# Performance work log

Measured on AMD Instinct MI355X. Metric: run time of the kernel, lower is better.

Reference implementation:

```python
import jax, jax.numpy as jnp
import numpy as np

N_NODES = 50000


def setup_inputs() -> dict:
    key = jax.random.key(0)
    ks = jax.random.split(key, 9)
    d = 256
    E = 800000
    inp = {
        "x": jax.random.normal(ks[0], (N_NODES, d), dtype=jnp.float32),
        "edge_index": jax.random.randint(ks[1], (2, E), 0, N_NODES, dtype=jnp.int64),
    }
    # 3 GCNConv layers, each: weight [in, out] and bias [out] (Glorot-ish scale)
    scale = 1.0 / np.sqrt(d)
    for i in range(3):
        inp[f"W{i+1}"] = jax.random.normal(ks[2 + 2 * i], (d, d), dtype=jnp.float32) * scale
        inp[f"b{i+1}"] = jnp.zeros((d,), dtype=jnp.float32)
    return inp


def _gcn_conv(h, src, dst, norm, W, b, n_nodes):
    # linear transform then normalized gather-scatter aggregation
    h = h @ W                                   # [N, out]
    msg = h[src] * norm[:, None]                # [E+N, out]
    out = jax.ops.segment_sum(msg, dst, num_segments=n_nodes)
    return out + b


def reference(x, edge_index, W1, b1, W2, b2, W3, b3):
    n = x.shape[0]
    loop = jnp.arange(n, dtype=edge_index.dtype)
    src = jnp.concatenate([edge_index[0], loop])  # add self-loops
    dst = jnp.concatenate([edge_index[1], loop])
    # symmetric normalization: deg^{-1/2}[src] * deg^{-1/2}[dst]
    deg = jax.ops.segment_sum(jnp.ones_like(dst, dtype=x.dtype), dst, num_segments=n)
    dinv = jnp.where(deg > 0, jax.lax.rsqrt(deg), 0.0)
    norm = dinv[src] * dinv[dst]

    h = _gcn_conv(x, src, dst, norm, W1, b1, n)
    h = jax.nn.relu(h)
    h = _gcn_conv(h, src, dst, norm, W2, b2, n)
    h = jax.nn.relu(h)
    h = _gcn_conv(h, src, dst, norm, W3, b3, n)
    return h
```

## Files before the change

kernel.cpp:

```cpp
#include <hip/hip_runtime.h>
#include <math.h>


using bf16x8  = __attribute__((ext_vector_type(8))) short;
using ushort4v = __attribute__((ext_vector_type(4))) unsigned short;
using f32x4   = __attribute__((ext_vector_type(4))) float;
using half4   = __attribute__((ext_vector_type(4))) _Float16;

__device__ inline unsigned short f2bf(float v) {
    union { float f; unsigned u; } x; x.f = v;
    unsigned r = x.u + 0x7fff + ((x.u >> 16) & 1);
    return (unsigned short)(r >> 16);
}
__device__ inline float bf2f(unsigned short b) {
    union { float f; unsigned u; } x; x.u = ((unsigned)b) << 16;
    return x.f;
}
__device__ inline unsigned short f2h_bits(float v) {
    _Float16 h = (_Float16)v;
    union { _Float16 h; unsigned short u; } c; c.h = h;
    return c.u;
}


__global__ void hist_kernel(const int* __restrict__ dst, int E, int* __restrict__ cnt) {
    int e = blockIdx.x * blockDim.x + threadIdx.x;
    if (e < E) atomicAdd(&cnt[dst[e]], 1);
}

__global__ void scan_block_kernel(const int* __restrict__ in, int n,
                                  int* __restrict__ out, int* __restrict__ bsums) {
    __shared__ int s[256];
    int t = threadIdx.x;
    int i = blockIdx.x * 256 + t;
    s[t] = (i < n) ? in[i] : 0;
    __syncthreads();
    for (int off = 1; off < 256; off <<= 1) {
        int addv = (t >= off) ? s[t - off] : 0;
        __syncthreads();
        s[t] += addv;
        __syncthreads();
    }
    if (i < n) out[i] = s[t];
    if (t == 255) bsums[blockIdx.x] = s[255];
}

__global__ void scan_sums_kernel(int* __restrict__ bsums, int nb) {
    __shared__ int s[256];
    int t = threadIdx.x;
    s[t] = (t < nb) ? bsums[t] : 0;
    __syncthreads();
    for (int off = 1; off < 256; off <<= 1) {
        int addv = (t >= off) ? s[t - off] : 0;
        __syncthreads();
        s[t] += addv;
        __syncthreads();
    }
    if (t < nb) bsums[t] = s[t];
}

__global__ void scan_add_dinv_kernel(int* __restrict__ scn, int n, const int* __restrict__ bsums,
                                     const int* __restrict__ cnt, float* __restrict__ dinv,
                                     int* __restrict__ cursor) {
    int i = blockIdx.x * 256 + threadIdx.x;
    if (i < n) {
        int s = scn[i] + (blockIdx.x > 0 ? bsums[blockIdx.x - 1] : 0);
        scn[i] = s;
        int c = cnt[i];
        dinv[i] = rsqrtf((float)(c + 1));
        cursor[i] = s - c;
    }
}

__global__ void scatter_kernel(const int* __restrict__ src, const int* __restrict__ dst, int E,
                               const float* __restrict__ dinv, int* __restrict__ cursor,
                               int* __restrict__ ssrc, float* __restrict__ snorm) {
    int e = blockIdx.x * blockDim.x + threadIdx.x;
    if (e < E) {
        int s = src[e], d0 = dst[e];
        int pos = atomicAdd(&cursor[d0], 1);
        ssrc[pos] = s;
        snorm[pos] = dinv[s] * dinv[d0];
    }
}

__global__ __launch_bounds__(256) void wsplit3_kernel(const float* __restrict__ Wa,
                                                      const float* __restrict__ Wb,
                                                      const float* __restrict__ Wc,
                                                      unsigned short* __restrict__ Wsp) {
    __shared__ float t[64][65];
    int w = blockIdx.z;
    const float* W = (w == 0) ? Wa : (w == 1) ? Wb : Wc;
    int k0 = blockIdx.x * 64, n0 = blockIdx.y * 64;
    int tid = threadIdx.x;
    int r = tid >> 6, c = tid & 63;
#pragma unroll
    for (int i = 0; i < 16; ++i) {
        int kk = i * 4 + r;
        t[kk][c] = W[(size_t)(k0 + kk) * 256 + n0 + c];
    }
    __syncthreads();
    unsigned short* Hi = Wsp + (size_t)w * 131072;
    unsigned short* Lo = Hi + 65536;
#pragma unroll
    for (int i = 0; i < 16; ++i) {
        int nn = i * 4 + r;
        float v = t[c][nn];
        unsigned short h = f2bf(v);
        unsigned short l2 = f2bf(v - bf2f(h));
        Hi[(size_t)(n0 + nn) * 256 + k0 + c] = h;
        Lo[(size_t)(n0 + nn) * 256 + k0 + c] = l2;
    }
}

__global__ void xsplit_kernel(const float* __restrict__ in, unsigned short* __restrict__ hi,
                              unsigned short* __restrict__ lo, int total4) {
    int i = blockIdx.x * blockDim.x + threadIdx.x;
    int stride = gridDim.x * blockDim.x;
    for (; i < total4; i += stride) {
        float4 v = ((const float4*)in)[i];
        ushort4v h, l;
        h[0] = f2bf(v.x); l[0] = f2bf(v.x - bf2f(h[0]));
        h[1] = f2bf(v.y); l[1] = f2bf(v.y - bf2f(h[1]));
        h[2] = f2bf(v.z); l[2] = f2bf(v.z - bf2f(h[2]));
        h[3] = f2bf(v.w); l[3] = f2bf(v.w - bf2f(h[3]));
        ((ushort4v*)hi)[i] = h;
        ((ushort4v*)lo)[i] = l;
    }
}

__global__ __launch_bounds__(256) void gemm_ps_kernel(
        const unsigned short* __restrict__ Ahi, const unsigned short* __restrict__ Alo,
        const unsigned short* __restrict__ Bht, const unsigned short* __restrict__ Blt,
        unsigned short* __restrict__ C16, int M) {
    __shared__ unsigned short lds[32768];

    const int tid  = threadIdx.x;
    const int lane = tid & 63;
    const int wid  = tid >> 6;
    const int wr   = wid >> 1, wc = wid & 1;

    const int orig = blockIdx.x;
    const int xcd  = orig & 7;
    const int idx  = orig >> 3;
    const int wg   = (xcd < 6 ? xcd * 98 : 588 + (xcd - 6) * 97) + idx;
    const int mBase = (wg >> 1) * 128;
    const int nBase = (wg & 1) * 128;

    const int b0 = (lane ^ (lane >> 2) ^ (lane >> 4)) & 1;
    const int b1 = ((lane >> 1) ^ (lane >> 3)) & 1;
    const int b2 = ((lane >> 2) ^ (lane >> 4)) & 1;
    const int g  = (lane & 0x38) | (b2 << 2) | (b1 << 1) | b0;
    const int srow = g >> 2;
    const int skg  = g & 3;

    const unsigned short* gbase =
        (wid == 0) ? Ahi : (wid == 1) ? Alo : (wid == 2) ? Bht : Blt;
    const int rowbase = (wid < 2) ? mBase : nBase;

    int grows[8];
#pragma unroll
    for (int c = 0; c < 8; ++c) {
        int r = rowbase + c * 16 + srow;
        if (wid < 2 && r >= M) r = M - 1;
        grows[c] = r;
    }

    f32x4 acc[4][4];
#pragma unroll
    for (int i = 0; i < 4; ++i)
#pragma unroll
        for (int j = 0; j < 4; ++j) acc[i][j] = (f32x4){0.f, 0.f, 0.f, 0.f};

    auto stage = [&](int p, int k) {
        unsigned short* ldsw = lds + p * 16384 + wid * 4096;
        const int k0 = k * 32;
#pragma unroll
        for (int c = 0; c < 8; ++c) {
            const unsigned short* ga = gbase + (size_t)grows[c] * 256 + k0 + skg * 8;
            __builtin_amdgcn_global_load_lds(
                (const __attribute__((address_space(1))) void*)ga,
                (__attribute__((address_space(3))) void*)(ldsw + c * 512),
                16, 0, 0);
        }
    };

    stage(0, 0);

#pragma unroll
    for (int k = 0; k < 8; ++k) {
        const int p = k & 1;
        if (k < 7) {
            stage(p ^ 1, k + 1);
            asm volatile("s_waitcnt vmcnt(8)" ::: "memory");
        } else {
            asm volatile("s_waitcnt vmcnt(0)" ::: "memory");
        }
        __builtin_amdgcn_s_barrier();

        const unsigned short* Ah = lds + p * 16384;
        const unsigned short* Al = Ah + 4096;
        const unsigned short* Bh = Ah + 8192;
        const unsigned short* Bl = Ah + 12288;

        const int kb = (lane >> 4) * 8;
        bf16x8 fah[4], fal[4], fbh[4], fbl[4];
#pragma unroll
        for (int mi = 0; mi < 4; ++mi) {
            int row = wr * 64 + mi * 16 + (lane & 15);
            int off = (row * 64 + kb * 2) ^ ((row & 7) << 4);
            fah[mi] = *(const bf16x8*)((const char*)Ah + off);
            fal[mi] = *(const bf16x8*)((const char*)Al + off);
        }
#pragma unroll
        for (int ni = 0; ni < 4; ++ni) {
            int col = wc * 64 + ni * 16 + (lane & 15);
            int off = (col * 64 + kb * 2) ^ ((col & 7) << 4);
            fbh[ni] = *(const bf16x8*)((const char*)Bh + off);
            fbl[ni] = *(const bf16x8*)((const char*)Bl + off);
        }
#pragma unroll
        for (int mi = 0; mi < 4; ++mi)
#pragma unroll
            for (int ni = 0; ni < 4; ++ni) {
                acc[mi][ni] = __builtin_amdgcn_mfma_f32_16x16x32_bf16(
                    fah[mi], fbh[ni], acc[mi][ni], 0, 0, 0);
                acc[mi][ni] = __builtin_amdgcn_mfma_f32_16x16x32_bf16(
                    fah[mi], fbl[ni], acc[mi][ni], 0, 0, 0);
                acc[mi][ni] = __builtin_amdgcn_mfma_f32_16x16x32_bf16(
                    fal[mi], fbh[ni], acc[mi][ni], 0, 0, 0);
            }
        __builtin_amdgcn_s_barrier();
    }

#pragma unroll
    for (int mi = 0; mi < 4; ++mi) {
        int row0 = mBase + wr * 64 + mi * 16 + (lane >> 4) * 4;
#pragma unroll
        for (int ni = 0; ni < 4; ++ni) {
            int col = nBase + wc * 64 + ni * 16 + (lane & 15);
#pragma unroll
            for (int r = 0; r < 4; ++r) {
                int row = row0 + r;
                if (row < M) C16[(size_t)row * 256 + col] = f2h_bits(acc[mi][ni][r]);
            }
        }
    }
}

template <int RELU, int SPLIT>
__global__ __launch_bounds__(256) void agg_kernel(const unsigned short* __restrict__ hH,
                                                  const int* __restrict__ ssrc,
                                                  const float* __restrict__ snorm,
                                                  const int* __restrict__ cnt,
                                                  const int* __restrict__ scanv,
                                                  const float* __restrict__ dinv,
                                                  const float* __restrict__ bias,
                                                  unsigned short* __restrict__ outHi,
                                                  unsigned short* __restrict__ outLo,
                                                  float* __restrict__ outF, int n) {
    int node = blockIdx.x * 4 + (threadIdx.x >> 6);
    int lane = threadIdx.x & 63;
    if (node >= n) return;
    int end = scanv[node];
    int start = end - cnt[node];
    float di = dinv[node];
    float wself = di * di;

    half4 v = ((const half4*)(hH + (size_t)node * 256))[lane];
    float ax = (float)v[0] * wself, ay = (float)v[1] * wself;
    float az = (float)v[2] * wself, aw = (float)v[3] * wself;

    int j = start;
    for (; j + 4 <= end; j += 4) {
        int s0 = ssrc[j], s1 = ssrc[j + 1], s2 = ssrc[j + 2], s3 = ssrc[j + 3];
        float w0 = snorm[j], w1 = snorm[j + 1], w2 = snorm[j + 2], w3 = snorm[j + 3];
        half4 u0 = ((const half4*)(hH + (size_t)s0 * 256))[lane];
        half4 u1 = ((const half4*)(hH + (size_t)s1 * 256))[lane];
        half4 u2 = ((const half4*)(hH + (size_t)s2 * 256))[lane];
        half4 u3 = ((const half4*)(hH + (size_t)s3 * 256))[lane];
        ax = fmaf((float)u0[0], w0, ax); ay = fmaf((float)u0[1], w0, ay);
        az = fmaf((float)u0[2], w0, az); aw = fmaf((float)u0[3], w0, aw);
        ax = fmaf((float)u1[0], w1, ax); ay = fmaf((float)u1[1], w1, ay);
        az = fmaf((float)u1[2], w1, az); aw = fmaf((float)u1[3], w1, aw);
        ax = fmaf((float)u2[0], w2, ax); ay = fmaf((float)u2[1], w2, ay);
        az = fmaf((float)u2[2], w2, az); aw = fmaf((float)u2[3], w2, aw);
        ax = fmaf((float)u3[0], w3, ax); ay = fmaf((float)u3[1], w3, ay);
        az = fmaf((float)u3[2], w3, az); aw = fmaf((float)u3[3], w3, aw);
    }
    for (; j < end; ++j) {
        int s = ssrc[j];
        float wn = snorm[j];
        half4 u = ((const half4*)(hH + (size_t)s * 256))[lane];
        ax = fmaf((float)u[0], wn, ax); ay = fmaf((float)u[1], wn, ay);
        az = fmaf((float)u[2], wn, az); aw = fmaf((float)u[3], wn, aw);
    }

    float4 bb = ((const float4*)bias)[lane];
    ax += bb.x; ay += bb.y; az += bb.z; aw += bb.w;
    if (RELU) {
        ax = fmaxf(ax, 0.0f); ay = fmaxf(ay, 0.0f);
        az = fmaxf(az, 0.0f); aw = fmaxf(aw, 0.0f);
    }
    if (SPLIT) {
        ushort4v h, l;
        h[0] = f2bf(ax); l[0] = f2bf(ax - bf2f(h[0]));
        h[1] = f2bf(ay); l[1] = f2bf(ay - bf2f(h[1]));
        h[2] = f2bf(az); l[2] = f2bf(az - bf2f(h[2]));
        h[3] = f2bf(aw); l[3] = f2bf(aw - bf2f(h[3]));
        ((ushort4v*)(outHi + (size_t)node * 256))[lane] = h;
        ((ushort4v*)(outLo + (size_t)node * 256))[lane] = l;
    } else {
        float4 o = {ax, ay, az, aw};
        ((float4*)(outF + (size_t)node * 256))[lane] = o;
    }
}

extern "C" void kernel_launch(void* const* d_in, const int* in_sizes, int n_in,
                              void* d_out, int out_size, void* d_ws, size_t ws_size,
                              hipStream_t stream) {
    const float* x  = (const float*)d_in[0];
    const int*   ei = (const int*)d_in[1];
    const float* W1 = (const float*)d_in[2];
    const float* b1 = (const float*)d_in[3];
    const float* W2 = (const float*)d_in[4];
    const float* b2 = (const float*)d_in[5];
    const float* W3 = (const float*)d_in[6];
    const float* b3 = (const float*)d_in[7];

    const int n = in_sizes[0] / 256;
    const int E = in_sizes[1] / 2;
    const int* src = ei;
    const int* dst = ei + E;

    unsigned short* Hi = (unsigned short*)d_out;
    unsigned short* Lo = Hi + (size_t)n * 256;
    float* outF = (float*)d_out;

    char* ws = (char*)d_ws;
    unsigned short* hH = (unsigned short*)ws;
    size_t off  = (size_t)n * 256 * 2;
    off = (off + 255) & ~(size_t)255;
    float* dinv = (float*)(ws + off); off += (size_t)n * 4;
    int*   cnt  = (int*)(ws + off);   off += (size_t)n * 4;
    int*   scn  = (int*)(ws + off);   off += (size_t)n * 4;
    int*   cur  = (int*)(ws + off);   off += (size_t)n * 4;
    int*   bsum = (int*)(ws + off);   off += 4096;
    int*   ssrc = (int*)(ws + off);   off += (size_t)E * 4;
    float* snrm = (float*)(ws + off); off += (size_t)E * 4;
    off = (off + 255) & ~(size_t)255;
    unsigned short* Wsp = (unsigned short*)(ws + off);
    off += (size_t)3 * 2 * 65536 * 2;

    hipMemsetAsync(cnt, 0, (size_t)n * 4, stream);

    const int eb = (E + 255) / 256;
    const int nb = (n + 255) / 256;

    wsplit3_kernel<<<dim3(4, 4, 3), 256, 0, stream>>>(W1, W2, W3, Wsp);
    xsplit_kernel<<<2048, 256, 0, stream>>>(x, Hi, Lo, n * 64);

    hist_kernel<<<eb, 256, 0, stream>>>(dst, E, cnt);
    scan_block_kernel<<<nb, 256, 0, stream>>>(cnt, n, scn, bsum);
    scan_sums_kernel<<<1, 256, 0, stream>>>(bsum, nb);
    scan_add_dinv_kernel<<<nb, 256, 0, stream>>>(scn, n, bsum, cnt, dinv, cur);
    scatter_kernel<<<eb, 256, 0, stream>>>(src, dst, E, dinv, cur, ssrc, snrm);

    const int gb = ((n + 127) / 128) * 2;
    const int ab = (n + 3) / 4;

    gemm_ps_kernel<<<gb, 256, 0, stream>>>(Hi, Lo, Wsp, Wsp + 65536, hH, n);
    agg_kernel<1, 1><<<ab, 256, 0, stream>>>(hH, ssrc, snrm, cnt, scn, dinv, b1,
                                             Hi, Lo, nullptr, n);
    gemm_ps_kernel<<<gb, 256, 0, stream>>>(Hi, Lo, Wsp + 131072, Wsp + 196608, hH, n);
    agg_kernel<1, 1><<<ab, 256, 0, stream>>>(hH, ssrc, snrm, cnt, scn, dinv, b2,
                                             Hi, Lo, nullptr, n);
    gemm_ps_kernel<<<gb, 256, 0, stream>>>(Hi, Lo, Wsp + 262144, Wsp + 327680, hH, n);
    agg_kernel<0, 0><<<ab, 256, 0, stream>>>(hH, ssrc, snrm, cnt, scn, dinv, b3,
                                             nullptr, nullptr, outF, n);
}
```

Baseline: 384.0 us.

## Switch GEMM to fp16 activations with split fp16 weights, dropping activation lo part

Replaces the bf16 hi/lo split of both activations and weights with a single fp16 activation operand and a hi/lo fp16 split of the weights only. This cuts the MFMA count per tile from three to two, cuts the LDS staging and global loads per k-step from eight to six, and halves the activation bytes written by the aggregation kernels and read by the GEMMs. The cost is precision: activations now carry fp16 precision and range instead of a near-fp32 split, which could exceed tolerance or overflow for large values.

```diff
diff --git a/kernel.cpp b/kernel.cpp
--- a/kernel.cpp
+++ b/kernel.cpp
@@ -2,20 +2,11 @@
 #include <math.h>
 
 
-using bf16x8  = __attribute__((ext_vector_type(8))) short;
+using f16x8   = __attribute__((ext_vector_type(8))) _Float16;
 using ushort4v = __attribute__((ext_vector_type(4))) unsigned short;
 using f32x4   = __attribute__((ext_vector_type(4))) float;
 using half4   = __attribute__((ext_vector_type(4))) _Float16;
 
-__device__ inline unsigned short f2bf(float v) {
-    union { float f; unsigned u; } x; x.f = v;
-    unsigned r = x.u + 0x7fff + ((x.u >> 16) & 1);
-    return (unsigned short)(r >> 16);
-}
-__device__ inline float bf2f(unsigned short b) {
-    union { float f; unsigned u; } x; x.u = ((unsigned)b) << 16;
-    return x.f;
-}
 __device__ inline unsigned short f2h_bits(float v) {
     _Float16 h = (_Float16)v;
     union { _Float16 h; unsigned short u; } c; c.h = h;
@@ -106,34 +97,32 @@
     for (int i = 0; i < 16; ++i) {
         int nn = i * 4 + r;
         float v = t[c][nn];
-        unsigned short h = f2bf(v);
-        unsigned short l2 = f2bf(v - bf2f(h));
-        Hi[(size_t)(n0 + nn) * 256 + k0 + c] = h;
-        Lo[(size_t)(n0 + nn) * 256 + k0 + c] = l2;
-    }
-}
-
-__global__ void xsplit_kernel(const float* __restrict__ in, unsigned short* __restrict__ hi,
-                              unsigned short* __restrict__ lo, int total4) {
+        _Float16 hh = (_Float16)v;
+        float rr = v - (float)hh;
+        _Float16 ll = (_Float16)rr;
+        union { _Float16 h; unsigned short u; } ch, cl; ch.h = hh; cl.h = ll;
+        Hi[(size_t)(n0 + nn) * 256 + k0 + c] = ch.u;
+        Lo[(size_t)(n0 + nn) * 256 + k0 + c] = cl.u;
+    }
+}
+
+__global__ void xcast_kernel(const float* __restrict__ in, unsigned short* __restrict__ out16,
+                             int total4) {
     int i = blockIdx.x * blockDim.x + threadIdx.x;
     int stride = gridDim.x * blockDim.x;
     for (; i < total4; i += stride) {
         float4 v = ((const float4*)in)[i];
-        ushort4v h, l;
-        h[0] = f2bf(v.x); l[0] = f2bf(v.x - bf2f(h[0]));
-        h[1] = f2bf(v.y); l[1] = f2bf(v.y - bf2f(h[1]));
-        h[2] = f2bf(v.z); l[2] = f2bf(v.z - bf2f(h[2]));
-        h[3] = f2bf(v.w); l[3] = f2bf(v.w - bf2f(h[3]));
-        ((ushort4v*)hi)[i] = h;
-        ((ushort4v*)lo)[i] = l;
-    }
-}
-
-__global__ __launch_bounds__(256) void gemm_ps_kernel(
-        const unsigned short* __restrict__ Ahi, const unsigned short* __restrict__ Alo,
-        const unsigned short* __restrict__ Bht, const unsigned short* __restrict__ Blt,
-        unsigned short* __restrict__ C16, int M) {
-    __shared__ unsigned short lds[32768];
+        ushort4v o;
+        o[0] = f2h_bits(v.x); o[1] = f2h_bits(v.y);
+        o[2] = f2h_bits(v.z); o[3] = f2h_bits(v.w);
+        ((ushort4v*)out16)[i] = o;
+    }
+}
+
+__global__ __launch_bounds__(256) void gemm_f16_kernel(
+        const unsigned short* __restrict__ Af, const unsigned short* __restrict__ Whf,
+        const unsigned short* __restrict__ Wlf, unsigned short* __restrict__ C16, int M) {
+    __shared__ unsigned short lds[24576];
 
     const int tid  = threadIdx.x;
     const int lane = tid & 63;
@@ -154,16 +143,19 @@
     const int srow = g >> 2;
     const int skg  = g & 3;
 
-    const unsigned short* gbase =
-        (wid == 0) ? Ahi : (wid == 1) ? Alo : (wid == 2) ? Bht : Blt;
-    const int rowbase = (wid < 2) ? mBase : nBase;
-
-    int grows[8];
-#pragma unroll
-    for (int c = 0; c < 8; ++c) {
-        int r = rowbase + c * 16 + srow;
-        if (wid < 2 && r >= M) r = M - 1;
-        grows[c] = r;
+    const unsigned short* cptr[6];
+    int cdst[6];
+#pragma unroll
+    for (int i = 0; i < 6; ++i) {
+        int c = wid * 6 + i;
+        int a = c >> 3;
+        int s = c & 7;
+        const unsigned short* base = (a == 0) ? Af : (a == 1) ? Whf : Wlf;
+        int rb = (a == 0) ? mBase : nBase;
+        int r = rb + s * 16 + srow;
+        if (a == 0 && r >= M) r = M - 1;
+        cptr[i] = base + (size_t)r * 256 + skg * 8;
+        cdst[i] = a * 4096 + s * 512;
     }
 
     f32x4 acc[4][4];
@@ -173,14 +165,13 @@
         for (int j = 0; j < 4; ++j) acc[i][j] = (f32x4){0.f, 0.f, 0.f, 0.f};
 
     auto stage = [&](int p, int k) {
-        unsigned short* ldsw = lds + p * 16384 + wid * 4096;
+        unsigned short* dbase = lds + p * 12288;
         const int k0 = k * 32;
 #pragma unroll
-        for (int c = 0; c < 8; ++c) {
-            const unsigned short* ga = gbase + (size_t)grows[c] * 256 + k0 + skg * 8;
+        for (int i = 0; i < 6; ++i) {
             __builtin_amdgcn_global_load_lds(
-                (const __attribute__((address_space(1))) void*)ga,
-                (__attribute__((address_space(3))) void*)(ldsw + c * 512),
+                (const __attribute__((address_space(1))) void*)(cptr[i] + k0),
+                (__attribute__((address_space(3))) void*)(dbase + cdst[i]),
                 16, 0, 0);
         }
     };
@@ -192,43 +183,39 @@
         const int p = k & 1;
         if (k < 7) {
             stage(p ^ 1, k + 1);
-            asm volatile("s_waitcnt vmcnt(8)" ::: "memory");
+            asm volatile("s_waitcnt vmcnt(6)" ::: "memory");
         } else {
             asm volatile("s_waitcnt vmcnt(0)" ::: "memory");
         }
         __builtin_amdgcn_s_barrier();
 
-        const unsigned short* Ah = lds + p * 16384;
-        const unsigned short* Al = Ah + 4096;
-        const unsigned short* Bh = Ah + 8192;
-        const unsigned short* Bl = Ah + 12288;
+        const unsigned short* As = lds + p * 12288;
+        const unsigned short* Bh = As + 4096;
+        const unsigned short* Bl = As + 8192;
 
         const int kb = (lane >> 4) * 8;
-        bf16x8 fah[4], fal[4], fbh[4], fbl[4];
+        f16x8 fa[4], fbh[4], fbl[4];
 #pragma unroll
         for (int mi = 0; mi < 4; ++mi) {
             int row = wr * 64 + mi * 16 + (lane & 15);
             int off = (row * 64 + kb * 2) ^ ((row & 7) << 4);
-            fah[mi] = *(const bf16x8*)((const char*)Ah + off);
-            fal[mi] = *(const bf16x8*)((const char*)Al + off);
+            fa[mi] = *(const f16x8*)((const char*)As + off);
         }
 #pragma unroll
         for (int ni = 0; ni < 4; ++ni) {
             int col = wc * 64 + ni * 16 + (lane & 15);
             int off = (col * 64 + kb * 2) ^ ((col & 7) << 4);
-            fbh[ni] = *(const bf16x8*)((const char*)Bh + off);
-            fbl[ni] = *(const bf16x8*)((const char*)Bl + off);
+            fbh[ni] = *(const f16x8*)((const char*)Bh + off);
+            fbl[ni] = *(const f16x8*)((const char*)Bl + off);
         }
 #pragma unroll
         for (int mi = 0; mi < 4; ++mi)
 #pragma unroll
             for (int ni = 0; ni < 4; ++ni) {
-                acc[mi][ni] = __builtin_amdgcn_mfma_f32_16x16x32_bf16(
-                    fah[mi], fbh[ni], acc[mi][ni], 0, 0, 0);
-                acc[mi][ni] = __builtin_amdgcn_mfma_f32_16x16x32_bf16(
-                    fah[mi], fbl[ni], acc[mi][ni], 0, 0, 0);
-                acc[mi][ni] = __builtin_amdgcn_mfma_f32_16x16x32_bf16(
-                    fal[mi], fbh[ni], acc[mi][ni], 0, 0, 0);
+                acc[mi][ni] = __builtin_amdgcn_mfma_f32_16x16x32_f16(
+                    fa[mi], fbh[ni], acc[mi][ni], 0, 0, 0);
+                acc[mi][ni] = __builtin_amdgcn_mfma_f32_16x16x32_f16(
+                    fa[mi], fbl[ni], acc[mi][ni], 0, 0, 0);
             }
         __builtin_amdgcn_s_barrier();
     }
@@ -256,8 +243,7 @@
                                                   const int* __restrict__ scanv,
                                                   const float* __restrict__ dinv,
                                                   const float* __restrict__ bias,
-                                                  unsigned short* __restrict__ outHi,
-                                                  unsigned short* __restrict__ outLo,
+                                                  unsigned short* __restrict__ outH,
                                                   float* __restrict__ outF, int n) {
     int node = blockIdx.x * 4 + (threadIdx.x >> 6);
     int lane = threadIdx.x & 63;
@@ -303,13 +289,10 @@
         az = fmaxf(az, 0.0f); aw = fmaxf(aw, 0.0f);
     }
     if (SPLIT) {
-        ushort4v h, l;
-        h[0] = f2bf(ax); l[0] = f2bf(ax - bf2f(h[0]));
-        h[1] = f2bf(ay); l[1] = f2bf(ay - bf2f(h[1]));
-        h[2] = f2bf(az); l[2] = f2bf(az - bf2f(h[2]));
-        h[3] = f2bf(aw); l[3] = f2bf(aw - bf2f(h[3]));
-        ((ushort4v*)(outHi + (size_t)node * 256))[lane] = h;
-        ((ushort4v*)(outLo + (size_t)node * 256))[lane] = l;
+        ushort4v o;
+        o[0] = f2h_bits(ax); o[1] = f2h_bits(ay);
+        o[2] = f2h_bits(az); o[3] = f2h_bits(aw);
+        ((ushort4v*)(outH + (size_t)node * 256))[lane] = o;
     } else {
         float4 o = {ax, ay, az, aw};
         ((float4*)(outF + (size_t)node * 256))[lane] = o;
@@ -333,12 +316,12 @@
     const int* src = ei;
     const int* dst = ei + E;
 
-    unsigned short* Hi = (unsigned short*)d_out;
-    unsigned short* Lo = Hi + (size_t)n * 256;
+    unsigned short* hAct = (unsigned short*)d_out;
+    unsigned short* xF   = hAct + (size_t)n * 256;
     float* outF = (float*)d_out;
 
     char* ws = (char*)d_ws;
-    unsigned short* hH = (unsigned short*)ws;
+    unsigned short* hLin = (unsigned short*)ws;
     size_t off  = (size_t)n * 256 * 2;
     off = (off + 255) & ~(size_t)255;
     float* dinv = (float*)(ws + off); off += (size_t)n * 4;
@@ -358,7 +341,7 @@
     const int nb = (n + 255) / 256;
 
     wsplit3_kernel<<<dim3(4, 4, 3), 256, 0, stream>>>(W1, W2, W3, Wsp);
-    xsplit_kernel<<<2048, 256, 0, stream>>>(x, Hi, Lo, n * 64);
+    xcast_kernel<<<2048, 256, 0, stream>>>(x, xF, n * 64);
 
     hist_kernel<<<eb, 256, 0, stream>>>(dst, E, cnt);
     scan_block_kernel<<<nb, 256, 0, stream>>>(cnt, n, scn, bsum);
@@ -369,13 +352,13 @@
     const int gb = ((n + 127) / 128) * 2;
     const int ab = (n + 3) / 4;
 
-    gemm_ps_kernel<<<gb, 256, 0, stream>>>(Hi, Lo, Wsp, Wsp + 65536, hH, n);
-    agg_kernel<1, 1><<<ab, 256, 0, stream>>>(hH, ssrc, snrm, cnt, scn, dinv, b1,
-                                             Hi, Lo, nullptr, n);
-    gemm_ps_kernel<<<gb, 256, 0, stream>>>(Hi, Lo, Wsp + 131072, Wsp + 196608, hH, n);
-    agg_kernel<1, 1><<<ab, 256, 0, stream>>>(hH, ssrc, snrm, cnt, scn, dinv, b2,
-                                             Hi, Lo, nullptr, n);
-    gemm_ps_kernel<<<gb, 256, 0, stream>>>(Hi, Lo, Wsp + 262144, Wsp + 327680, hH, n);
-    agg_kernel<0, 0><<<ab, 256, 0, stream>>>(hH, ssrc, snrm, cnt, scn, dinv, b3,
-                                             nullptr, nullptr, outF, n);
-}
+    gemm_f16_kernel<<<gb, 256, 0, stream>>>(xF, Wsp, Wsp + 65536, hLin, n);
+    agg_kernel<1, 1><<<ab, 256, 0, stream>>>(hLin, ssrc, snrm, cnt, scn, dinv, b1,
+                                             hAct, nullptr, n);
+    gemm_f16_kernel<<<gb, 256, 0, stream>>>(hAct, Wsp + 131072, Wsp + 196608, hLin, n);
+    agg_kernel<1, 1><<<ab, 256, 0, stream>>>(hLin, ssrc, snrm, cnt, scn, dinv, b2,
+                                             hAct, nullptr, n);
+    gemm_f16_kernel<<<gb, 256, 0, stream>>>(hAct, Wsp + 262144, Wsp + 327680, hLin, n);
+    agg_kernel<0, 0><<<ab, 256, 0, stream>>>(hLin, ssrc, snrm, cnt, scn, dinv, b3,
+                                             nullptr, outF, n);
+}
```

After: 355.1 us. 1.08x faster.
